# Kernel tuning notes

Hardware: AMD Instinct MI355X
Metric: run time of the kernel (lower is better)

The kernel has to match this reference:

```python
import jax, jax.numpy as jnp
import numpy as np

M, K, N, GS = 64, 4096, 14336, 128
# pack() interleaves every block of 8 k-columns with perm [0,2,4,6,1,3,5,7];
# nibble i of a packed int32 holds original column 8*c + PERM[i].
PERM = np.array([0, 2, 4, 6, 1, 3, 5, 7])
INV_PERM = np.argsort(PERM)  # [0,4,1,5,2,6,3,7]


def setup_inputs() -> dict:
    key = jax.random.key(0)
    k1, k2, k3 = jax.random.split(key, 3)
    x = jax.random.normal(k1, (M, K), dtype=jnp.float32)
    B_packed = jax.random.randint(k2, (N, K // 8), 0, 2147483647, dtype=jnp.int32)
    # positive per-group scales (typical magnitude for 4-bit symmetric quant)
    s = jax.random.uniform(k3, (K // GS, N), dtype=jnp.float32) * 0.02 + 1e-3
    return {"x": x, "B_packed": B_packed, "s": s}


def _dequantize(B_packed, s):
    # Unpack 8 nibbles per int32 -> (N, K//8, 8)
    u = B_packed.astype(jnp.uint32)
    nibs = jnp.stack([(u >> (4 * i)) & 0xF for i in range(8)], axis=-1)
    # Undo the pack-time column interleave within each block of 8
    nibs = nibs[..., jnp.asarray(INV_PERM)]
    q = nibs.reshape(N, K).astype(jnp.float32) - 8.0  # symmetric int4: values in [-8, 7]
    # Apply per-group, per-output-channel scales: s[k//GS, n]
    w = (q.reshape(N, K // GS, GS) * s.T[:, :, None]).reshape(N, K)  # (N, K)
    return w


def reference(x, B_packed, s):
    w = _dequantize(B_packed, s)        # (N, K) dequantized fp32 weight
    return jnp.einsum("mk,nk->mn", x, w)  # (M, N), no bias
```

## Files before the change

### kernel.cpp

```cpp
#include <hip/hip_runtime.h>
#include <stdint.h>

typedef _Float16 f16;
typedef f16   f16x2 __attribute__((ext_vector_type(2)));
typedef f16   f16x8 __attribute__((ext_vector_type(8)));
typedef float f32x4 __attribute__((ext_vector_type(4)));

static constexpr int M_ = 64;
static constexpr int K_ = 4096;
static constexpr int N_ = 14336;

__global__ void xconv_kernel(const float* __restrict__ x, uint4* __restrict__ xt) {
    int t = blockIdx.x * blockDim.x + threadIdx.x;
    int row = t >> 9, kb = t & 511;
    int kg = kb >> 2, h = kb & 3, mt = row >> 4, l16 = row & 15;
    int dst = (kg * 4 + mt) * 64 + h * 16 + l16;
    const float4* p = reinterpret_cast<const float4*>(x) + 2 * (size_t)t;
    float4 a = p[0], b = p[1];
    union { f16x8 h8; uint4 v; } z;
    z.h8[0] = (f16)a.x; z.h8[1] = (f16)a.y; z.h8[2] = (f16)a.z; z.h8[3] = (f16)a.w;
    z.h8[4] = (f16)b.x; z.h8[5] = (f16)b.y; z.h8[6] = (f16)b.z; z.h8[7] = (f16)b.w;
    xt[dst] = z.v;
}

__device__ __forceinline__ f16x8 dequant(uint u, f16x2 sc) {
    const f16 m = (f16)(-1032.0f);
    const f16x2 mc = {m, m};
    union { f16x2 h2; uint uu; } um;
    union { f16x2 h2[4]; f16x8 v; } ob;
    #pragma unroll
    for (int p = 0; p < 4; ++p) {
        um.uu = 0x64006400u | ((u >> (4 * p)) & 0x000F000Fu);
        ob.h2[p] = (um.h2 + mc) * sc;
    }
    return ob.v;
}

template<bool PRE>
__global__ __launch_bounds__(512, 4)
void gemm_kernel(const float* __restrict__ xf, const f16x8* __restrict__ xt8,
                 const uint* __restrict__ bpk, const float* __restrict__ s,
                 float* __restrict__ out)
{
    __shared__ __align__(16) uint lbs[16384];
    const int tid  = threadIdx.x;
    const int lane = tid & 63;
    const int w    = tid >> 6;
    const int h    = lane >> 4;
    const int l16  = lane & 15;
    const int n0   = blockIdx.x * 32;

    f16x2 sc0[4], sc1[4];
    #pragma unroll
    for (int g = 0; g < 4; ++g) {
        float a = s[(size_t)(w * 4 + g) * N_ + n0 + l16];
        float b = s[(size_t)(w * 4 + g) * N_ + n0 + 16 + l16];
        f16 ha = (f16)a, hb = (f16)b;
        sc0[g] = f16x2{ha, ha};
        sc1[g] = f16x2{hb, hb};
    }

#define LOADB(G, R0, R1)                                                              \
    {                                                                                 \
        const uint* p0_ = bpk + (size_t)(n0 +      l16) * 512 + w * 64 + (G) * 16 + h * 4; \
        const uint* p1_ = bpk + (size_t)(n0 + 16 + l16) * 512 + w * 64 + (G) * 16 + h * 4; \
        R0 = *reinterpret_cast<const uint4*>(p0_);                                    \
        R1 = *reinterpret_cast<const uint4*>(p1_);                                    \
    }
#define WRITEB(BUF, R0, R1)                                                           \
    {                                                                                 \
        uint4* d_ = reinterpret_cast<uint4*>(lbs + w * 1024 + (BUF) * 512) + lane;    \
        d_[0] = R0; d_[64] = R1;                                                      \
    }
#define LOADA(DST, KS, MT)                                                                         \
    if constexpr (PRE) { DST = xt8[(size_t)(((w * 16 + (KS)) * 4 + (MT)) * 64 + lane)]; }          \
    else {                                                                                         \
        const float* xp_ = xf + (size_t)((MT) * 16 + l16) * K_ + (size_t)(w * 16 + (KS)) * 32 + h * 8; \
        float4 f0_ = *reinterpret_cast<const float4*>(xp_);                                        \
        float4 f1_ = *reinterpret_cast<const float4*>(xp_ + 4);                                    \
        f16x8 av_;                                                                                 \
        av_[0] = (f16)f0_.x; av_[1] = (f16)f0_.y; av_[2] = (f16)f0_.z; av_[3] = (f16)f0_.w;        \
        av_[4] = (f16)f1_.x; av_[5] = (f16)f1_.y; av_[6] = (f16)f1_.z; av_[7] = (f16)f1_.w;        \
        DST = av_;                                                                                 \
    }

    uint4 tE0, tE1, tO0, tO1;
    LOADB(0, tE0, tE1)
    LOADB(1, tO0, tO1)
    WRITEB(0, tE0, tE1)

    f16x8 ap[2][4];
    #pragma unroll
    for (int mt = 0; mt < 4; ++mt) { LOADA(ap[0][mt], 0, mt) }
    #pragma unroll
    for (int mt = 0; mt < 4; ++mt) { LOADA(ap[1][mt], 1, mt) }

    f32x4 acc[2][4];
    #pragma unroll
    for (int nt = 0; nt < 2; ++nt)
        #pragma unroll
        for (int mt = 0; mt < 4; ++mt) acc[nt][mt] = f32x4{0.f, 0.f, 0.f, 0.f};

#define COMPUTE_T(G, T, U0, U1)                                                           \
    {                                                                                     \
        const f16x8 a0_ = ap[((G) * 4 + (T)) & 1][0];                                     \
        const f16x8 a1_ = ap[((G) * 4 + (T)) & 1][1];                                     \
        const f16x8 a2_ = ap[((G) * 4 + (T)) & 1][2];                                     \
        const f16x8 a3_ = ap[((G) * 4 + (T)) & 1][3];                                     \
        if ((G) * 4 + (T) + 2 < 16) {                                                     \
            LOADA(ap[((G) * 4 + (T)) & 1][0], (G) * 4 + (T) + 2, 0)                       \
            LOADA(ap[((G) * 4 + (T)) & 1][1], (G) * 4 + (T) + 2, 1)                       \
            LOADA(ap[((G) * 4 + (T)) & 1][2], (G) * 4 + (T) + 2, 2)                       \
            LOADA(ap[((G) * 4 + (T)) & 1][3], (G) * 4 + (T) + 2, 3)                       \
        }                                                                                 \
        const f16x8 b0_ = dequant(U0, sc0[(G)]);                                          \
        const f16x8 b1_ = dequant(U1, sc1[(G)]);                                          \
        acc[0][0] = __builtin_amdgcn_mfma_f32_16x16x32_f16(a0_, b0_, acc[0][0], 0, 0, 0); \
        acc[0][1] = __builtin_amdgcn_mfma_f32_16x16x32_f16(a1_, b0_, acc[0][1], 0, 0, 0); \
        acc[0][2] = __builtin_amdgcn_mfma_f32_16x16x32_f16(a2_, b0_, acc[0][2], 0, 0, 0); \
        acc[0][3] = __builtin_amdgcn_mfma_f32_16x16x32_f16(a3_, b0_, acc[0][3], 0, 0, 0); \
        acc[1][0] = __builtin_amdgcn_mfma_f32_16x16x32_f16(a0_, b1_, acc[1][0], 0, 0, 0); \
        acc[1][1] = __builtin_amdgcn_mfma_f32_16x16x32_f16(a1_, b1_, acc[1][1], 0, 0, 0); \
        acc[1][2] = __builtin_amdgcn_mfma_f32_16x16x32_f16(a2_, b1_, acc[1][2], 0, 0, 0); \
        acc[1][3] = __builtin_amdgcn_mfma_f32_16x16x32_f16(a3_, b1_, acc[1][3], 0, 0, 0); \
    }

#define GROUP(G, WBUF, WR0, WR1, DOWRITE)                                             \
    {                                                                                 \
        const int rb_ = w * 1024 + ((G) & 1) * 512 + l16 * 4 + h;                     \
        const uint u00_ = lbs[rb_ +   0], u01_ = lbs[rb_ +  64];                      \
        const uint u02_ = lbs[rb_ + 128], u03_ = lbs[rb_ + 192];                      \
        const uint u10_ = lbs[rb_ + 256], u11_ = lbs[rb_ + 320];                      \
        const uint u12_ = lbs[rb_ + 384], u13_ = lbs[rb_ + 448];                      \
        COMPUTE_T(G, 0, u00_, u10_)                                                   \
        if (DOWRITE) { WRITEB(WBUF, WR0, WR1) }                                       \
        COMPUTE_T(G, 1, u01_, u11_)                                                   \
        COMPUTE_T(G, 2, u02_, u12_)                                                   \
        COMPUTE_T(G, 3, u03_, u13_)                                                   \
    }

    { LOADB(2, tE0, tE1) }
    GROUP(0, 1, tO0, tO1, true)
    { LOADB(3, tO0, tO1) }
    GROUP(1, 0, tE0, tE1, true)
    GROUP(2, 1, tO0, tO1, true)
    GROUP(3, 0, tE0, tE1, false)

#undef GROUP
#undef COMPUTE_T
#undef LOADA
#undef WRITEB
#undef LOADB

    __syncthreads();
    f32x4* red = reinterpret_cast<f32x4*>(lbs);
    #pragma unroll
    for (int nt = 0; nt < 2; ++nt)
        #pragma unroll
        for (int mt = 0; mt < 4; ++mt)
            red[(w * 8 + nt * 4 + mt) * 64 + lane] = acc[nt][mt];
    __syncthreads();
    {
        f32x4 v = red[(0 * 8 + w) * 64 + lane];
        v += red[(1 * 8 + w) * 64 + lane];
        v += red[(2 * 8 + w) * 64 + lane];
        v += red[(3 * 8 + w) * 64 + lane];
        v += red[(4 * 8 + w) * 64 + lane];
        v += red[(5 * 8 + w) * 64 + lane];
        v += red[(6 * 8 + w) * 64 + lane];
        v += red[(7 * 8 + w) * 64 + lane];
        const int nt = w >> 2, mt = w & 3;
        #pragma unroll
        for (int q = 0; q < 4; ++q)
            out[(size_t)(mt * 16 + h * 4 + q) * N_ + (n0 + nt * 16 + l16)] = v[q];
    }
}

extern "C" void kernel_launch(void* const* d_in, const int* in_sizes, int n_in,
                              void* d_out, int out_size, void* d_ws, size_t ws_size,
                              hipStream_t stream) {
    const float* x   = (const float*)d_in[0];
    const uint*  bpk = (const uint*)d_in[1];
    const float* s   = (const float*)d_in[2];
    float*       out = (float*)d_out;

    if (ws_size >= (size_t)(M_ * K_ * 2)) {
        xconv_kernel<<<128, 256, 0, stream>>>(x, (uint4*)d_ws);
        gemm_kernel<true><<<448, 512, 0, stream>>>(x, (const f16x8*)d_ws, bpk, s, out);
    } else {
        gemm_kernel<false><<<448, 512, 0, stream>>>(x, nullptr, bpk, s, out);
    }
}
```

Measured before the change: 24.96 us.

## Widen per-block N tile to 64 columns and halve grid size

Each workgroup now covers 64 output columns instead of 32, loading four B rows per lane and issuing 16 MFMAs per k-step. Each A fragment loaded from the converted-x buffer is therefore reused across twice as many columns, which halves total A traffic. The grid shrinks from 448 to 224 blocks and launch bounds drop to 2 waves/EU to make room for the extra registers. This leaves fewer blocks than the 256 CUs on MI355X, so some CUs sit idle, and the cross-wave reduction now runs in two passes.

Result: slower. 27.72 us (+11.1%).

```diff
diff --git a/kernel.cpp b/kernel.cpp
--- a/kernel.cpp
+++ b/kernel.cpp
@@ -37,7 +37,7 @@
 }
 
 template<bool PRE>
-__global__ __launch_bounds__(512, 4)
+__global__ __launch_bounds__(512, 2)
 void gemm_kernel(const float* __restrict__ xf, const f16x8* __restrict__ xt8,
                  const uint* __restrict__ bpk, const float* __restrict__ s,
                  float* __restrict__ out)
@@ -48,29 +48,31 @@
     const int w    = tid >> 6;
     const int h    = lane >> 4;
     const int l16  = lane & 15;
-    const int n0   = blockIdx.x * 32;
-
-    f16x2 sc0[4], sc1[4];
+    const int n0   = blockIdx.x * 64;
+
+    f16x2 sc0[4], sc1[4], sc2[4], sc3[4];
     #pragma unroll
     for (int g = 0; g < 4; ++g) {
-        float a = s[(size_t)(w * 4 + g) * N_ + n0 + l16];
-        float b = s[(size_t)(w * 4 + g) * N_ + n0 + 16 + l16];
-        f16 ha = (f16)a, hb = (f16)b;
-        sc0[g] = f16x2{ha, ha};
-        sc1[g] = f16x2{hb, hb};
-    }
-
-#define LOADB(G, R0, R1)                                                              \
+        const size_t gb = (size_t)(w * 4 + g) * N_ + n0 + l16;
+        f16 a0 = (f16)s[gb], a1 = (f16)s[gb + 16], a2 = (f16)s[gb + 32], a3 = (f16)s[gb + 48];
+        sc0[g] = f16x2{a0, a0};
+        sc1[g] = f16x2{a1, a1};
+        sc2[g] = f16x2{a2, a2};
+        sc3[g] = f16x2{a3, a3};
+    }
+
+#define LOADB(G, R0, R1, R2, R3)                                                      \
     {                                                                                 \
-        const uint* p0_ = bpk + (size_t)(n0 +      l16) * 512 + w * 64 + (G) * 16 + h * 4; \
-        const uint* p1_ = bpk + (size_t)(n0 + 16 + l16) * 512 + w * 64 + (G) * 16 + h * 4; \
-        R0 = *reinterpret_cast<const uint4*>(p0_);                                    \
-        R1 = *reinterpret_cast<const uint4*>(p1_);                                    \
-    }
-#define WRITEB(BUF, R0, R1)                                                           \
+        const size_t bb_ = (size_t)(n0 + l16) * 512 + w * 64 + (G) * 16 + h * 4;      \
+        R0 = *reinterpret_cast<const uint4*>(bpk + bb_);                              \
+        R1 = *reinterpret_cast<const uint4*>(bpk + bb_ + 16 * 512);                   \
+        R2 = *reinterpret_cast<const uint4*>(bpk + bb_ + 32 * 512);                   \
+        R3 = *reinterpret_cast<const uint4*>(bpk + bb_ + 48 * 512);                   \
+    }
+#define WRITEB(BUF, R0, R1, R2, R3)                                                   \
     {                                                                                 \
-        uint4* d_ = reinterpret_cast<uint4*>(lbs + w * 1024 + (BUF) * 512) + lane;    \
-        d_[0] = R0; d_[64] = R1;                                                      \
+        uint4* d_ = reinterpret_cast<uint4*>(lbs + w * 2048 + (BUF) * 1024) + lane;   \
+        d_[0] = R0; d_[64] = R1; d_[128] = R2; d_[192] = R3;                          \
     }
 #define LOADA(DST, KS, MT)                                                                         \
     if constexpr (PRE) { DST = xt8[(size_t)(((w * 16 + (KS)) * 4 + (MT)) * 64 + lane)]; }          \
@@ -84,10 +86,10 @@
         DST = av_;                                                                                 \
     }
 
-    uint4 tE0, tE1, tO0, tO1;
-    LOADB(0, tE0, tE1)
-    LOADB(1, tO0, tO1)
-    WRITEB(0, tE0, tE1)
+    uint4 tE0, tE1, tE2, tE3, tO0, tO1, tO2, tO3;
+    LOADB(0, tE0, tE1, tE2, tE3)
+    LOADB(1, tO0, tO1, tO2, tO3)
+    WRITEB(0, tE0, tE1, tE2, tE3)
 
     f16x8 ap[2][4];
     #pragma unroll
@@ -95,13 +97,13 @@
     #pragma unroll
     for (int mt = 0; mt < 4; ++mt) { LOADA(ap[1][mt], 1, mt) }
 
-    f32x4 acc[2][4];
-    #pragma unroll
-    for (int nt = 0; nt < 2; ++nt)
+    f32x4 acc[4][4];
+    #pragma unroll
+    for (int nt = 0; nt < 4; ++nt)
         #pragma unroll
         for (int mt = 0; mt < 4; ++mt) acc[nt][mt] = f32x4{0.f, 0.f, 0.f, 0.f};
 
-#define COMPUTE_T(G, T, U0, U1)                                                           \
+#define COMPUTE_T(G, T, U0, U1, U2, U3)                                                   \
     {                                                                                     \
         const f16x8 a0_ = ap[((G) * 4 + (T)) & 1][0];                                     \
         const f16x8 a1_ = ap[((G) * 4 + (T)) & 1][1];                                     \
@@ -115,6 +117,8 @@
         }                                                                                 \
         const f16x8 b0_ = dequant(U0, sc0[(G)]);                                          \
         const f16x8 b1_ = dequant(U1, sc1[(G)]);                                          \
+        const f16x8 b2_ = dequant(U2, sc2[(G)]);                                          \
+        const f16x8 b3_ = dequant(U3, sc3[(G)]);                                          \
         acc[0][0] = __builtin_amdgcn_mfma_f32_16x16x32_f16(a0_, b0_, acc[0][0], 0, 0, 0); \
         acc[0][1] = __builtin_amdgcn_mfma_f32_16x16x32_f16(a1_, b0_, acc[0][1], 0, 0, 0); \
         acc[0][2] = __builtin_amdgcn_mfma_f32_16x16x32_f16(a2_, b0_, acc[0][2], 0, 0, 0); \
@@ -123,28 +127,40 @@
         acc[1][1] = __builtin_amdgcn_mfma_f32_16x16x32_f16(a1_, b1_, acc[1][1], 0, 0, 0); \
         acc[1][2] = __builtin_amdgcn_mfma_f32_16x16x32_f16(a2_, b1_, acc[1][2], 0, 0, 0); \
         acc[1][3] = __builtin_amdgcn_mfma_f32_16x16x32_f16(a3_, b1_, acc[1][3], 0, 0, 0); \
-    }
-
-#define GROUP(G, WBUF, WR0, WR1, DOWRITE)                                             \
+        acc[2][0] = __builtin_amdgcn_mfma_f32_16x16x32_f16(a0_, b2_, acc[2][0], 0, 0, 0); \
+        acc[2][1] = __builtin_amdgcn_mfma_f32_16x16x32_f16(a1_, b2_, acc[2][1], 0, 0, 0); \
+        acc[2][2] = __builtin_amdgcn_mfma_f32_16x16x32_f16(a2_, b2_, acc[2][2], 0, 0, 0); \
+        acc[2][3] = __builtin_amdgcn_mfma_f32_16x16x32_f16(a3_, b2_, acc[2][3], 0, 0, 0); \
+        acc[3][0] = __builtin_amdgcn_mfma_f32_16x16x32_f16(a0_, b3_, acc[3][0], 0, 0, 0); \
+        acc[3][1] = __builtin_amdgcn_mfma_f32_16x16x32_f16(a1_, b3_, acc[3][1], 0, 0, 0); \
+        acc[3][2] = __builtin_amdgcn_mfma_f32_16x16x32_f16(a2_, b3_, acc[3][2], 0, 0, 0); \
+        acc[3][3] = __builtin_amdgcn_mfma_f32_16x16x32_f16(a3_, b3_, acc[3][3], 0, 0, 0); \
+    }
+
+#define GROUP(G, WBUF, W0, W1, W2, W3, DOWRITE)                                       \
     {                                                                                 \
-        const int rb_ = w * 1024 + ((G) & 1) * 512 + l16 * 4 + h;                     \
+        const int rb_ = w * 2048 + ((G) & 1) * 1024 + l16 * 4 + h;                    \
         const uint u00_ = lbs[rb_ +   0], u01_ = lbs[rb_ +  64];                      \
         const uint u02_ = lbs[rb_ + 128], u03_ = lbs[rb_ + 192];                      \
         const uint u10_ = lbs[rb_ + 256], u11_ = lbs[rb_ + 320];                      \
         const uint u12_ = lbs[rb_ + 384], u13_ = lbs[rb_ + 448];                      \
-        COMPUTE_T(G, 0, u00_, u10_)                                                   \
-        if (DOWRITE) { WRITEB(WBUF, WR0, WR1) }                                       \
-        COMPUTE_T(G, 1, u01_, u11_)                                                   \
-        COMPUTE_T(G, 2, u02_, u12_)                                                   \
-        COMPUTE_T(G, 3, u03_, u13_)                                                   \
-    }
-
-    { LOADB(2, tE0, tE1) }
-    GROUP(0, 1, tO0, tO1, true)
-    { LOADB(3, tO0, tO1) }
-    GROUP(1, 0, tE0, tE1, true)
-    GROUP(2, 1, tO0, tO1, true)
-    GROUP(3, 0, tE0, tE1, false)
+        const uint u20_ = lbs[rb_ + 512], u21_ = lbs[rb_ + 576];                      \
+        const uint u22_ = lbs[rb_ + 640], u23_ = lbs[rb_ + 704];                      \
+        const uint u30_ = lbs[rb_ + 768], u31_ = lbs[rb_ + 832];                      \
+        const uint u32_ = lbs[rb_ + 896], u33_ = lbs[rb_ + 960];                      \
+        COMPUTE_T(G, 0, u00_, u10_, u20_, u30_)                                       \
+        if (DOWRITE) { WRITEB(WBUF, W0, W1, W2, W3) }                                 \
+        COMPUTE_T(G, 1, u01_, u11_, u21_, u31_)                                       \
+        COMPUTE_T(G, 2, u02_, u12_, u22_, u32_)                                       \
+        COMPUTE_T(G, 3, u03_, u13_, u23_, u33_)                                       \
+    }
+
+    { LOADB(2, tE0, tE1, tE2, tE3) }
+    GROUP(0, 1, tO0, tO1, tO2, tO3, true)
+    { LOADB(3, tO0, tO1, tO2, tO3) }
+    GROUP(1, 0, tE0, tE1, tE2, tE3, true)
+    GROUP(2, 1, tO0, tO1, tO2, tO3, true)
+    GROUP(3, 0, tE0, tE1, tE2, tE3, false)
 
 #undef GROUP
 #undef COMPUTE_T
@@ -152,27 +168,30 @@
 #undef WRITEB
 #undef LOADB
 
-    __syncthreads();
     f32x4* red = reinterpret_cast<f32x4*>(lbs);
     #pragma unroll
-    for (int nt = 0; nt < 2; ++nt)
+    for (int pass = 0; pass < 2; ++pass) {
+        __syncthreads();
         #pragma unroll
-        for (int mt = 0; mt < 4; ++mt)
-            red[(w * 8 + nt * 4 + mt) * 64 + lane] = acc[nt][mt];
-    __syncthreads();
-    {
-        f32x4 v = red[(0 * 8 + w) * 64 + lane];
-        v += red[(1 * 8 + w) * 64 + lane];
-        v += red[(2 * 8 + w) * 64 + lane];
-        v += red[(3 * 8 + w) * 64 + lane];
-        v += red[(4 * 8 + w) * 64 + lane];
-        v += red[(5 * 8 + w) * 64 + lane];
-        v += red[(6 * 8 + w) * 64 + lane];
-        v += red[(7 * 8 + w) * 64 + lane];
-        const int nt = w >> 2, mt = w & 3;
-        #pragma unroll
-        for (int q = 0; q < 4; ++q)
-            out[(size_t)(mt * 16 + h * 4 + q) * N_ + (n0 + nt * 16 + l16)] = v[q];
+        for (int nl = 0; nl < 2; ++nl)
+            #pragma unroll
+            for (int mt = 0; mt < 4; ++mt)
+                red[(w * 8 + nl * 4 + mt) * 64 + lane] = acc[pass * 2 + nl][mt];
+        __syncthreads();
+        {
+            f32x4 v = red[(0 * 8 + w) * 64 + lane];
+            v += red[(1 * 8 + w) * 64 + lane];
+            v += red[(2 * 8 + w) * 64 + lane];
+            v += red[(3 * 8 + w) * 64 + lane];
+            v += red[(4 * 8 + w) * 64 + lane];
+            v += red[(5 * 8 + w) * 64 + lane];
+            v += red[(6 * 8 + w) * 64 + lane];
+            v += red[(7 * 8 + w) * 64 + lane];
+            const int nt = pass * 2 + (w >> 2), mt = w & 3;
+            #pragma unroll
+            for (int q = 0; q < 4; ++q)
+                out[(size_t)(mt * 16 + h * 4 + q) * N_ + (n0 + nt * 16 + l16)] = v[q];
+        }
     }
 }
 
@@ -186,8 +205,8 @@
 
     if (ws_size >= (size_t)(M_ * K_ * 2)) {
         xconv_kernel<<<128, 256, 0, stream>>>(x, (uint4*)d_ws);
-        gemm_kernel<true><<<448, 512, 0, stream>>>(x, (const f16x8*)d_ws, bpk, s, out);
+        gemm_kernel<true><<<224, 512, 0, stream>>>(x, (const f16x8*)d_ws, bpk, s, out);
     } else {
-        gemm_kernel<false><<<448, 512, 0, stream>>>(x, nullptr, bpk, s, out);
-    }
-}
+        gemm_kernel<false><<<224, 512, 0, stream>>>(x, nullptr, bpk, s, out);
+    }
+}
```
